# Kernel optimization log

Measured on AMD Instinct MI355X. Metric: run time of the kernel, lower is better.

## Reference

```python
import jax, jax.numpy as jnp
import numpy as np
import jax.scipy.linalg as jsl

K = 4           # num_hops + 1
N = 4096        # nodes
D = 256         # in_dim == out_dim
S = 32          # subspace_dim
ETA = 0.5
EPS = 0.5


def setup_inputs() -> dict:
    key = jax.random.key(0)
    k1, k2, k3 = jax.random.split(key, 3)
    hops = jax.random.normal(k1, (K, N, D), dtype=jnp.float32)
    A = (jax.random.uniform(k2, (N, N)) < 0.01).astype(jnp.float32)
    A = jnp.maximum(A, A.T)
    A = jnp.fill_diagonal(A, 1.0, inplace=False)
    deg = A.sum(axis=1)
    L = jnp.diag(deg) - A  # graph Laplacian
    # orthonormal subspace bases via QR, as in __init__
    raw = jax.random.normal(k3, (K, D, S), dtype=jnp.float32)
    q, _ = jnp.linalg.qr(raw)
    U = q[:, :, :S]
    hop_weights = jnp.ones((K,), dtype=jnp.float32) / K
    threshold = jnp.full((D,), 0.05, dtype=jnp.float32)
    lambda_lap = jnp.asarray(0.1, dtype=jnp.float32)
    return {"hops": hops, "adj_mask": A, "L": L, "U": U,
            "hop_weights": hop_weights, "threshold": threshold,
            "lambda_lap": lambda_lap}


def reference(hops, adj_mask, L, U, hop_weights, threshold, lambda_lap):
    n = hops.shape[1]
    s = U.shape[-1]
    w = jax.nn.softmax(hop_weights, axis=0)
    mask_add = (1.0 - adj_mask) * -1e9  # [n, n]
    I_s = jnp.eye(s, dtype=hops.dtype)
    agg_total = jnp.zeros((hops.shape[2], n), dtype=hops.dtype)  # [d, n]
    coeff = s / (n * EPS ** 2)
    for k in range(K):  # small fixed hop count
        Uk = U[k]                      # [d, s]
        Zk = Uk.T @ hops[k].T          # [s, n]
        M_k = I_s + coeff * (Zk @ Zk.T)  # [s, s]
        cf = jsl.cho_factor(M_k)
        M_inv = jsl.cho_solve(cf, I_s)   # Cholesky inverse
        MZ = M_inv @ Zk                  # [s, n]
        scores = Zk.T @ MZ + mask_add    # [n, n] Mahalanobis-style attention
        alpha = jax.nn.softmax(scores, axis=1)
        grad_k = Uk @ (MZ @ alpha.T)     # [d, n]
        agg_total = agg_total + w[k] * grad_k
    H_agg = agg_total.T                  # [n, d]
    lap_grad = lambda_lap * (L @ H_agg)
    H_half = hops[0] + ETA * H_agg - ETA * lap_grad
    # soft-threshold (proximal step); in_dim == out_dim so no proj
    H_out = jnp.sign(H_half) * jax.nn.relu(jnp.abs(H_half) - threshold[None, :])
    # orthogonality regularizer over subspace bases
    orth_loss = jnp.asarray(0.0, dtype=hops.dtype)
    for k in range(K):
        UkTUk = U[k].T @ U[k]
        orth_loss = orth_loss + ((UkTUk - I_s) ** 2).sum()
        for l in range(k + 1, K):
            orth_loss = orth_loss + ((U[k].T @ U[l]) ** 2).sum()
    lap_smooth = jnp.sum(H_out * (L @ H_out))  # trace(H^T L H)
    return (H_out, orth_loss, lap_smooth, jax.lax.stop_gradient(w))
```

## Files before the change

kernel.cpp:

```cpp
#include <hip/hip_runtime.h>
#include <cstddef>

typedef unsigned short ushortt;
typedef unsigned int uintt;

static constexpr int Nn = 4096;
static constexpr int Dd = 256;
static constexpr int Ss = 32;
static constexpr int Kk = 4;
static constexpr int CAP = 144;
static constexpr int RST = 136;
static constexpr float kEta   = 0.5f;
static constexpr float kCoeff = 0.03125f;

__device__ __forceinline__ float waveReduceSum(float v){
  #pragma unroll
  for (int off = 32; off > 0; off >>= 1) v += __shfl_down(v, off, 64);
  return v;
}
__device__ __forceinline__ float blo(uintt u){ return __uint_as_float(u << 16); }
__device__ __forceinline__ float bhi(uintt u){ return __uint_as_float(u & 0xffff0000u); }
__device__ __forceinline__ ushortt f2b(float x){
  uintt u = __float_as_uint(x);
  uintt r = (u + 0x7fffu + ((u >> 16) & 1u)) >> 16;
  return (ushortt)r;
}
__device__ __forceinline__ float b2f(ushortt u){ return __uint_as_float(((uintt)u) << 16); }

__global__ __launch_bounds__(256) void build_kernel(const float* __restrict__ A,
                                                    const float* __restrict__ hw,
                                                    int* __restrict__ deg,
                                                    int* __restrict__ colx,
                                                    float* __restrict__ out){
  int i = blockIdx.x, tid = threadIdx.x;
  if (i == 0 && tid == 0){
    out[1048576] = 0.f;
    out[1048577] = 0.f;
    float a0=hw[0], a1=hw[1], a2=hw[2], a3=hw[3];
    float mx = fmaxf(fmaxf(a0,a1), fmaxf(a2,a3));
    float e0=expf(a0-mx), e1=expf(a1-mx), e2=expf(a2-mx), e3=expf(a3-mx);
    float s = e0+e1+e2+e3;
    out[1048578]=e0/s; out[1048579]=e1/s; out[1048580]=e2/s; out[1048581]=e3/s;
  }
  int lane = tid & 63, w = tid >> 6;
  __shared__ int wbuf[4][96];
  __shared__ int wcnt[4];
  const float4* row4 = (const float4*)(A + (size_t)i * Nn);
  int cnt = 0;
  int base = w * 256;
  unsigned long long below = (lane == 63) ? 0x7fffffffffffffffull : ((1ull << lane) - 1ull);
  #pragma unroll
  for (int it = 0; it < 4; it++){
    int c4 = base + it * 64 + lane;
    float4 v = row4[c4];
    bool f0 = (v.x != 0.f), f1 = (v.y != 0.f), f2 = (v.z != 0.f), f3 = (v.w != 0.f);
    unsigned long long m0 = __ballot(f0), m1 = __ballot(f1),
                       m2 = __ballot(f2), m3 = __ballot(f3);
    int pre = __popcll(m0 & below) + __popcll(m1 & below)
            + __popcll(m2 & below) + __popcll(m3 & below);
    int pos = cnt + pre;
    int j0 = c4 * 4;
    if (f0){ if (pos < 96) wbuf[w][pos] = j0;     pos++; }
    if (f1){ if (pos < 96) wbuf[w][pos] = j0 + 1; pos++; }
    if (f2){ if (pos < 96) wbuf[w][pos] = j0 + 2; pos++; }
    if (f3){ if (pos < 96) wbuf[w][pos] = j0 + 3; pos++; }
    cnt += __popcll(m0) + __popcll(m1) + __popcll(m2) + __popcll(m3);
  }
  if (cnt > 96) cnt = 96;
  if (lane == 0) wcnt[w] = cnt;
  __syncthreads();
  int off = 0;
  for (int ww = 0; ww < w; ww++) off += wcnt[ww];
  int total = wcnt[0] + wcnt[1] + wcnt[2] + wcnt[3];
  for (int idx = lane; idx < cnt; idx += 64){
    int p = off + idx;
    if (p < CAP) colx[(size_t)i * CAP + p] = wbuf[w][idx];
  }
  if (tid == 0) deg[i] = (total < CAP) ? total : CAP;
}

__global__ __launch_bounds__(256) void z_kernel(const float* __restrict__ hops,
                                                const float* __restrict__ U,
                                                float* __restrict__ Zt4,
                                                float* __restrict__ Ubt){
  int b = blockIdx.x;
  int k = b >> 9;
  int i0 = (b & 511) * 8;
  __shared__ float Us[Ss][260];
  for (int t = threadIdx.x; t < Dd * Ss; t += 256){
    int s = t & 31, d = t >> 5;
    Us[s][d] = U[(size_t)k * Dd * Ss + t];
  }
  __syncthreads();
  int s = threadIdx.x & 31, ii = threadIdx.x >> 5;
  int i = i0 + ii;
  const float4* h4 = (const float4*)(hops + ((size_t)k * Nn + i) * Dd);
  const float4* u4 = (const float4*)(&Us[s][0]);
  float acc = 0.f;
  #pragma unroll 8
  for (int dq = 0; dq < 64; dq++){
    float4 h = h4[dq];
    float4 u = u4[dq];
    acc += h.x*u.x + h.y*u.y + h.z*u.z + h.w*u.w;
  }
  Zt4[(size_t)i * 128 + k * 32 + s] = acc;
  if (b < 128){
    int idx = b * 256 + threadIdx.x;
    int c = idx >> 8, d = idx & 255;
    int kk = c >> 5, s2 = c & 31;
    Ubt[idx] = U[(size_t)kk * Dd * Ss + (size_t)d * Ss + s2];
  }
}

__global__ __launch_bounds__(256) void mpart_kernel(const float* __restrict__ Zt4,
                                                    float* __restrict__ Mpart){
  int b = blockIdx.x;
  int k = b >> 4, ch = b & 15;
  int i0 = ch * 256;
  __shared__ float zs[256][33];
  for (int t = threadIdx.x; t < 256 * 32; t += 256){
    int ii = t >> 5, s = t & 31;
    zs[ii][s] = Zt4[(size_t)(i0 + ii) * 128 + k * 32 + s];
  }
  __syncthreads();
  int tid = threadIdx.x;
  int s2 = tid & 31, s1b = tid >> 5;
  float a0=0.f, a1=0.f, a2=0.f, a3=0.f;
  for (int ii = 0; ii < 256; ii++){
    float zc = zs[ii][s2];
    a0 = fmaf(zs[ii][s1b],      zc, a0);
    a1 = fmaf(zs[ii][8 + s1b],  zc, a1);
    a2 = fmaf(zs[ii][16 + s1b], zc, a2);
    a3 = fmaf(zs[ii][24 + s1b], zc, a3);
  }
  float* outp = Mpart + (size_t)b * 1024;
  outp[0 * 256 + tid] = a0;
  outp[1 * 256 + tid] = a1;
  outp[2 * 256 + tid] = a2;
  outp[3 * 256 + tid] = a3;
}

__global__ __launch_bounds__(256) void inv_kernel(const float* __restrict__ Mpart,
                                                  float* __restrict__ Minv){
  __shared__ float Msh[4][32][33];
  int tid = threadIdx.x;
  for (int e = tid; e < 4096; e += 256){
    int k = e >> 10, rc = e & 1023;
    float s = 0.f;
    for (int ch = 0; ch < 16; ch++) s += Mpart[(size_t)(k * 16 + ch) * 1024 + rc];
    int r = rc >> 5, c = rc & 31;
    Msh[k][r][c] = kCoeff * s + ((r == c) ? 1.f : 0.f);
  }
  __syncthreads();
  int k = tid >> 6, lane = tid & 63, r = lane & 31, half = lane >> 5;
  float a[32];
  #pragma unroll
  for (int j = 0; j < 32; j++) a[j] = half ? ((r == j) ? 1.f : 0.f) : Msh[k][r][j];
  #pragma unroll
  for (int p = 0; p < 32; p++){
    float app = __shfl(a[p], p, 64);
    float pinv = 1.f / app;
    float f = __shfl(a[p], r, 64);
    #pragma unroll
    for (int j = 0; j < 32; j++){
      float pr = __shfl(a[j], p + (half << 5), 64) * pinv;
      a[j] = (r == p) ? pr : fmaf(-f, pr, a[j]);
    }
  }
  if (half){
    #pragma unroll
    for (int j = 0; j < 32; j++) Minv[(size_t)k * 1024 + r * 32 + j] = a[j];
  }
}

__global__ __launch_bounds__(256) void mz_kernel(const float* __restrict__ Zt4,
                                                 const float* __restrict__ Minv,
                                                 ushortt* __restrict__ MZb){
  int b = blockIdx.x;
  int k = b >> 7;
  int i0 = (b & 127) * 32;
  __shared__ float mi[32][33];
  __shared__ float zs[32][33];
  for (int t = threadIdx.x; t < 1024; t += 256){
    int ii = t >> 5, s2 = t & 31;
    mi[ii][s2] = Minv[(size_t)k * 1024 + t];
    zs[ii][s2] = Zt4[(size_t)(i0 + ii) * 128 + k * 32 + s2];
  }
  __syncthreads();
  int s = threadIdx.x & 31;
  for (int rr = 0; rr < 4; rr++){
    int ii = rr * 8 + (threadIdx.x >> 5);
    float acc = 0.f;
    #pragma unroll
    for (int s2 = 0; s2 < 32; s2++) acc = fmaf(mi[s][s2], zs[ii][s2], acc);
    MZb[(size_t)(i0 + ii) * 128 + k * 32 + s] = f2b(acc);
  }
}

__global__ __launch_bounds__(256) void agg_kernel(const float* __restrict__ Zt4,
                                                  const ushortt* __restrict__ MZb,
                                                  const float* __restrict__ wvec,
                                                  const int* __restrict__ deg,
                                                  const int* __restrict__ colx,
                                                  float* __restrict__ Vw){
  int i = blockIdx.x, tid = threadIdx.x;
  int lane = tid & 63, k = tid >> 6;
  __shared__ __align__(16) ushortt rows[CAP * RST];
  __shared__ int cols[CAP];
  __shared__ __align__(16) float zi[128];
  __shared__ float sc[4][CAP + 8];
  int m = deg[i];
  if (tid < 128) zi[tid] = Zt4[(size_t)i * 128 + tid];
  if (tid < m)  cols[tid] = colx[(size_t)i * CAP + tid];
  __syncthreads();

  int q = tid & 3, r = tid >> 2;
  float zq[32];
  {
    const float4* z4 = (const float4*)(&zi[q * 32]);
    #pragma unroll
    for (int p = 0; p < 8; p++){
      float4 z = z4[p];
      zq[p*4+0]=z.x; zq[p*4+1]=z.y; zq[p*4+2]=z.z; zq[p*4+3]=z.w;
    }
  }

  for (int t = r; t < m; t += 64){
    int j = cols[t];
    const uint4* src = (const uint4*)(MZb + (size_t)j * 128 + q * 32);
    uint4 q0 = src[0], q1 = src[1], q2 = src[2], q3 = src[3];
    uint4* dst = (uint4*)(rows + (size_t)t * RST + q * 32);
    dst[0] = q0; dst[1] = q1; dst[2] = q2; dst[3] = q3;
    float acc = 0.f;
    acc += blo(q0.x)*zq[0] + bhi(q0.x)*zq[1] + blo(q0.y)*zq[2] + bhi(q0.y)*zq[3];
    acc += blo(q0.z)*zq[4] + bhi(q0.z)*zq[5] + blo(q0.w)*zq[6] + bhi(q0.w)*zq[7];
    acc += blo(q1.x)*zq[8] + bhi(q1.x)*zq[9] + blo(q1.y)*zq[10]+ bhi(q1.y)*zq[11];
    acc += blo(q1.z)*zq[12]+ bhi(q1.z)*zq[13]+ blo(q1.w)*zq[14]+ bhi(q1.w)*zq[15];
    acc += blo(q2.x)*zq[16]+ bhi(q2.x)*zq[17]+ blo(q2.y)*zq[18]+ bhi(q2.y)*zq[19];
    acc += blo(q2.z)*zq[20]+ bhi(q2.z)*zq[21]+ blo(q2.w)*zq[22]+ bhi(q2.w)*zq[23];
    acc += blo(q3.x)*zq[24]+ bhi(q3.x)*zq[25]+ blo(q3.y)*zq[26]+ bhi(q3.y)*zq[27];
    acc += blo(q3.z)*zq[28]+ bhi(q3.z)*zq[29]+ blo(q3.w)*zq[30]+ bhi(q3.w)*zq[31];
    sc[q][t] = acc;
  }
  __syncthreads();

  float lmax = -3.0e38f;
  for (int t = lane; t < m; t += 64) lmax = fmaxf(lmax, sc[k][t]);
  #pragma unroll
  for (int off = 32; off > 0; off >>= 1) lmax = fmaxf(lmax, __shfl_xor(lmax, off, 64));
  float lsum = 0.f;
  for (int t = lane; t < m; t += 64){
    float e = __expf(sc[k][t] - lmax);
    sc[k][t] = e;
    lsum += e;
  }
  #pragma unroll
  for (int off = 32; off > 0; off >>= 1) lsum += __shfl_xor(lsum, off, 64);
  float scale = wvec[k] / lsum;

  int c2 = lane & 15, h = lane >> 4;
  float a0 = 0.f, a1 = 0.f;
  #pragma unroll 4
  for (int t = h; t < m; t += 4){
    uintt u = *(const uintt*)(rows + (size_t)t * RST + k * 32 + c2 * 2);
    float e = sc[k][t];
    a0 = fmaf(blo(u), e, a0);
    a1 = fmaf(bhi(u), e, a1);
  }
  a0 += __shfl_xor(a0, 16, 64); a0 += __shfl_xor(a0, 32, 64);
  a1 += __shfl_xor(a1, 16, 64); a1 += __shfl_xor(a1, 32, 64);
  if (h == 0){
    float2 v2 = make_float2(a0 * scale, a1 * scale);
    *(float2*)(Vw + (size_t)i * 128 + k * 32 + c2 * 2) = v2;
  }
}

__global__ __launch_bounds__(256) void gatherv_kernel(const float* __restrict__ Vw,
                                                      const float* __restrict__ lam_ptr,
                                                      const int* __restrict__ deg,
                                                      const int* __restrict__ colx,
                                                      float* __restrict__ cVc){
  int i = blockIdx.x, tid = threadIdx.x;
  int c = tid & 127, g = tid >> 7;
  __shared__ int cols[CAP];
  __shared__ float vred[2][128];
  int m = deg[i];
  if (tid < m) cols[tid] = colx[(size_t)i * CAP + tid];
  __syncthreads();
  float acc = 0.f;
  #pragma unroll 8
  for (int t = g; t < m; t += 2)
    acc += Vw[(size_t)cols[t] * 128 + c];
  vred[g][c] = acc;
  __syncthreads();
  if (tid < 128){
    float nb = vred[0][tid] + vred[1][tid];
    float lam = lam_ptr[0];
    float self = Vw[(size_t)i * 128 + tid];
    cVc[(size_t)i * 128 + tid] = kEta * (1.f - lam * (float)m) * self + kEta * lam * nb;
  }
}

__global__ __launch_bounds__(256) void houtblend_kernel(const float* __restrict__ cVc,
                                                        const float* __restrict__ Ubt,
                                                        const float* __restrict__ hops0,
                                                        const float* __restrict__ thr,
                                                        const float* __restrict__ U,
                                                        float* __restrict__ out,
                                                        ushortt* __restrict__ Hb){
  int tid = threadIdx.x;
  if (blockIdx.x >= 256){
    int g = (blockIdx.x - 256) * 256 + tid;
    int pair = g >> 10;
    int idx = g & 1023;
    int s1 = idx >> 5, s2 = idx & 31;
    const int pk_[10] = {0,0,0,0,1,1,1,2,2,3};
    const int pl_[10] = {0,1,2,3,1,2,3,2,3,3};
    int pk = pk_[pair], pl = pl_[pair];
    const float* Uk = U + (size_t)pk * Dd * Ss;
    const float* Ul = U + (size_t)pl * Dd * Ss;
    float dot = 0.f;
    for (int d = 0; d < Dd; d++) dot += Uk[d * Ss + s1] * Ul[d * Ss + s2];
    float val = dot - ((pk == pl && s1 == s2) ? 1.f : 0.f);
    val *= val;
    val = waveReduceSum(val);
    __shared__ float redo[4];
    if ((tid & 63) == 0) redo[tid >> 6] = val;
    __syncthreads();
    if (tid == 0) atomicAdd(out + 1048576, redo[0] + redo[1] + redo[2] + redo[3]);
    return;
  }
  int i0 = blockIdx.x * 16;
  __shared__ float Cs[16][132];
  for (int t = tid; t < 16 * 128; t += 256){
    int ii = t >> 7, c = t & 127;
    Cs[ii][c] = cVc[(size_t)(i0 + ii) * 128 + c];
  }
  __syncthreads();
  int d4 = tid & 63, g = tid >> 6;
  float4 acc[4];
  #pragma unroll
  for (int r = 0; r < 4; r++) acc[r] = make_float4(0.f, 0.f, 0.f, 0.f);
  #pragma unroll 2
  for (int c = 0; c < 128; c++){
    float4 ub = ((const float4*)(Ubt + (size_t)c * 256))[d4];
    #pragma unroll
    for (int r = 0; r < 4; r++){
      float cs = Cs[g * 4 + r][c];
      acc[r].x = fmaf(cs, ub.x, acc[r].x);
      acc[r].y = fmaf(cs, ub.y, acc[r].y);
      acc[r].z = fmaf(cs, ub.z, acc[r].z);
      acc[r].w = fmaf(cs, ub.w, acc[r].w);
    }
  }
  float4 th = ((const float4*)thr)[d4];
  #pragma unroll
  for (int r = 0; r < 4; r++){
    int i = i0 + g * 4 + r;
    float4 hp = ((const float4*)(hops0 + (size_t)i * 256))[d4];
    float hx = hp.x + acc[r].x, hy = hp.y + acc[r].y;
    float hz = hp.z + acc[r].z, hw = hp.w + acc[r].w;
    float4 o;
    o.x = copysignf(fmaxf(fabsf(hx) - th.x, 0.f), hx);
    o.y = copysignf(fmaxf(fabsf(hy) - th.y, 0.f), hy);
    o.z = copysignf(fmaxf(fabsf(hz) - th.z, 0.f), hz);
    o.w = copysignf(fmaxf(fabsf(hw) - th.w, 0.f), hw);
    ((float4*)(out + (size_t)i * 256))[d4] = o;
    ushort4 hb;
    hb.x = f2b(o.x); hb.y = f2b(o.y); hb.z = f2b(o.z); hb.w = f2b(o.w);
    *((ushort4*)(Hb + (size_t)i * 256 + d4 * 4)) = hb;
  }
}

__global__ __launch_bounds__(256) void lap_kernel(const float* __restrict__ Hout,
                                                  const ushortt* __restrict__ Hb,
                                                  const int* __restrict__ deg,
                                                  const int* __restrict__ colx,
                                                  float* __restrict__ lap_part){
  int b = blockIdx.x;
  int i = b >> 1, half = b & 1;
  int tid = threadIdx.x;
  int dl = tid & 127, g = tid >> 7;
  int d = half * 128 + dl;
  __shared__ int cols[CAP];
  int m = deg[i];
  if (tid < m) cols[tid] = colx[(size_t)i * CAP + tid];
  __syncthreads();
  float nb = 0.f;
  #pragma unroll 8
  for (int t = g; t < m; t += 2)
    nb += b2f(Hb[(size_t)cols[t] * 256 + d]);
  float hi = Hout[(size_t)i * 256 + d];
  float part = -hi * nb;
  if (g == 0) part = fmaf((float)m * hi, hi, part);
  part = waveReduceSum(part);
  __shared__ float red[4];
  if ((tid & 63) == 0) red[tid >> 6] = part;
  __syncthreads();
  if (tid == 0) lap_part[b] = red[0] + red[1] + red[2] + red[3];
}

__global__ __launch_bounds__(256) void lapred_kernel(const float* __restrict__ lap_part,
                                                     float* __restrict__ out){
  int tid = threadIdx.x;
  float s = 0.f;
  const float4* p4 = (const float4*)lap_part;
  #pragma unroll
  for (int q = 0; q < 8; q++){
    float4 v = p4[q * 256 + tid];
    s += v.x + v.y + v.z + v.w;
  }
  s = waveReduceSum(s);
  __shared__ float red[4];
  if ((tid & 63) == 0) red[tid >> 6] = s;
  __syncthreads();
  if (tid == 0) out[1048577] = red[0] + red[1] + red[2] + red[3];
}

extern "C" void kernel_launch(void* const* d_in, const int* in_sizes, int n_in,
                              void* d_out, int out_size, void* d_ws, size_t ws_size,
                              hipStream_t stream)
{
  const float* hops = (const float*)d_in[0];
  const float* A    = (const float*)d_in[1];
  const float* L    = (const float*)d_in[2];
  const float* U    = (const float*)d_in[3];
  const float* hw   = (const float*)d_in[4];
  const float* thr  = (const float*)d_in[5];
  const float* lam  = (const float*)d_in[6];
  (void)L; (void)in_sizes; (void)n_in; (void)out_size; (void)ws_size;

  float* out = (float*)d_out;
  float* ws  = (float*)d_ws;

  float*   Zt4   = ws;
  float*   Vw    = ws + 524288;
  float*   cVc   = ws + 1048576;
  ushortt* MZb   = (ushortt*)(ws + 1572864);
  ushortt* Hb    = (ushortt*)(ws + 1835008);
  float*   Ubt   = ws + 2359296;
  float*   Mpart = ws + 2392064;
  float*   Minv  = ws + 2457600;
  int*     deg   = (int*)(ws + 2461696);
  int*     colx  = (int*)(ws + 2465792);
  float*   lapp  = ws + 3121152;

  float* w_out = out + 1048578;

  build_kernel    <<<Nn, 256, 0, stream>>>(A, hw, deg, colx, out);
  z_kernel        <<<Kk*512, 256, 0, stream>>>(hops, U, Zt4, Ubt);
  mpart_kernel    <<<Kk*16, 256, 0, stream>>>(Zt4, Mpart);
  inv_kernel      <<<1, 256, 0, stream>>>(Mpart, Minv);
  mz_kernel       <<<Kk*128, 256, 0, stream>>>(Zt4, Minv, MZb);
  agg_kernel      <<<Nn, 256, 0, stream>>>(Zt4, MZb, w_out, deg, colx, Vw);
  gatherv_kernel  <<<Nn, 256, 0, stream>>>(Vw, lam, deg, colx, cVc);
  houtblend_kernel<<<296, 256, 0, stream>>>(cVc, Ubt, hops, thr, U, out, Hb);
  lap_kernel      <<<2*Nn, 256, 0, stream>>>(out, Hb, deg, colx, lapp);
  lapred_kernel   <<<1, 256, 0, stream>>>(lapp, out);
}
```

Baseline: 303.2 us.

## Fuse build with Z projection, gather with blend, and lap reduction via last-block

Merges the adjacency-build and Z-projection kernels into one launch that splits work by block index. Folds the neighbor gather of Vw into the output blend kernel, so each block handles 4 rows and the cVc intermediate buffer is no longer needed. Replaces the separate lap reduction launch with an atomic done-counter that lets the last lap block do the final sum. This removes three kernel launches and one global round trip. In exchange the blend kernel runs with less per-block row reuse of Ubt and gets more blocks, and the reduction now relies on an atomic counter.

```diff
diff --git a/kernel.cpp b/kernel.cpp
--- a/kernel.cpp
+++ b/kernel.cpp
@@ -27,15 +27,52 @@
 }
 __device__ __forceinline__ float b2f(ushortt u){ return __uint_as_float(((uintt)u) << 16); }
 
-__global__ __launch_bounds__(256) void build_kernel(const float* __restrict__ A,
-                                                    const float* __restrict__ hw,
-                                                    int* __restrict__ deg,
-                                                    int* __restrict__ colx,
-                                                    float* __restrict__ out){
-  int i = blockIdx.x, tid = threadIdx.x;
+__global__ __launch_bounds__(256) void buildz_kernel(const float* __restrict__ A,
+                                                     const float* __restrict__ hw,
+                                                     const float* __restrict__ hops,
+                                                     const float* __restrict__ U,
+                                                     int* __restrict__ deg,
+                                                     int* __restrict__ colx,
+                                                     float* __restrict__ Zt4,
+                                                     float* __restrict__ Ubt,
+                                                     int* __restrict__ done_ctr,
+                                                     float* __restrict__ out){
+  int tid = threadIdx.x;
+  if (blockIdx.x >= Nn){
+    int b = blockIdx.x - Nn;
+    int k = b >> 9;
+    int i0 = (b & 511) * 8;
+    __shared__ float Us[Ss][260];
+    for (int t = tid; t < Dd * Ss; t += 256){
+      int s = t & 31, d = t >> 5;
+      Us[s][d] = U[(size_t)k * Dd * Ss + t];
+    }
+    __syncthreads();
+    int s = tid & 31, ii = tid >> 5;
+    int i = i0 + ii;
+    const float4* h4 = (const float4*)(hops + ((size_t)k * Nn + i) * Dd);
+    const float4* u4 = (const float4*)(&Us[s][0]);
+    float acc = 0.f;
+    #pragma unroll 8
+    for (int dq = 0; dq < 64; dq++){
+      float4 h = h4[dq];
+      float4 u = u4[dq];
+      acc += h.x*u.x + h.y*u.y + h.z*u.z + h.w*u.w;
+    }
+    Zt4[(size_t)i * 128 + k * 32 + s] = acc;
+    if (b < 128){
+      int idx = b * 256 + tid;
+      int c = idx >> 8, d = idx & 255;
+      int kk = c >> 5, s2 = c & 31;
+      Ubt[idx] = U[(size_t)kk * Dd * Ss + (size_t)d * Ss + s2];
+    }
+    return;
+  }
+  int i = blockIdx.x;
   if (i == 0 && tid == 0){
     out[1048576] = 0.f;
     out[1048577] = 0.f;
+    *done_ctr = 0;
     float a0=hw[0], a1=hw[1], a2=hw[2], a3=hw[3];
     float mx = fmaxf(fmaxf(a0,a1), fmaxf(a2,a3));
     float e0=expf(a0-mx), e1=expf(a1-mx), e2=expf(a2-mx), e3=expf(a3-mx);
@@ -77,39 +114,6 @@
     if (p < CAP) colx[(size_t)i * CAP + p] = wbuf[w][idx];
   }
   if (tid == 0) deg[i] = (total < CAP) ? total : CAP;
-}
-
-__global__ __launch_bounds__(256) void z_kernel(const float* __restrict__ hops,
-                                                const float* __restrict__ U,
-                                                float* __restrict__ Zt4,
-                                                float* __restrict__ Ubt){
-  int b = blockIdx.x;
-  int k = b >> 9;
-  int i0 = (b & 511) * 8;
-  __shared__ float Us[Ss][260];
-  for (int t = threadIdx.x; t < Dd * Ss; t += 256){
-    int s = t & 31, d = t >> 5;
-    Us[s][d] = U[(size_t)k * Dd * Ss + t];
-  }
-  __syncthreads();
-  int s = threadIdx.x & 31, ii = threadIdx.x >> 5;
-  int i = i0 + ii;
-  const float4* h4 = (const float4*)(hops + ((size_t)k * Nn + i) * Dd);
-  const float4* u4 = (const float4*)(&Us[s][0]);
-  float acc = 0.f;
-  #pragma unroll 8
-  for (int dq = 0; dq < 64; dq++){
-    float4 h = h4[dq];
-    float4 u = u4[dq];
-    acc += h.x*u.x + h.y*u.y + h.z*u.z + h.w*u.w;
-  }
-  Zt4[(size_t)i * 128 + k * 32 + s] = acc;
-  if (b < 128){
-    int idx = b * 256 + threadIdx.x;
-    int c = idx >> 8, d = idx & 255;
-    int kk = c >> 5, s2 = c & 31;
-    Ubt[idx] = U[(size_t)kk * Dd * Ss + (size_t)d * Ss + s2];
-  }
 }
 
 __global__ __launch_bounds__(256) void mpart_kernel(const float* __restrict__ Zt4,
@@ -275,42 +279,19 @@
   }
 }
 
-__global__ __launch_bounds__(256) void gatherv_kernel(const float* __restrict__ Vw,
-                                                      const float* __restrict__ lam_ptr,
-                                                      const int* __restrict__ deg,
-                                                      const int* __restrict__ colx,
-                                                      float* __restrict__ cVc){
-  int i = blockIdx.x, tid = threadIdx.x;
-  int c = tid & 127, g = tid >> 7;
-  __shared__ int cols[CAP];
-  __shared__ float vred[2][128];
-  int m = deg[i];
-  if (tid < m) cols[tid] = colx[(size_t)i * CAP + tid];
-  __syncthreads();
-  float acc = 0.f;
-  #pragma unroll 8
-  for (int t = g; t < m; t += 2)
-    acc += Vw[(size_t)cols[t] * 128 + c];
-  vred[g][c] = acc;
-  __syncthreads();
-  if (tid < 128){
-    float nb = vred[0][tid] + vred[1][tid];
-    float lam = lam_ptr[0];
-    float self = Vw[(size_t)i * 128 + tid];
-    cVc[(size_t)i * 128 + tid] = kEta * (1.f - lam * (float)m) * self + kEta * lam * nb;
-  }
-}
-
-__global__ __launch_bounds__(256) void houtblend_kernel(const float* __restrict__ cVc,
-                                                        const float* __restrict__ Ubt,
-                                                        const float* __restrict__ hops0,
-                                                        const float* __restrict__ thr,
-                                                        const float* __restrict__ U,
-                                                        float* __restrict__ out,
-                                                        ushortt* __restrict__ Hb){
+__global__ __launch_bounds__(256) void gho_kernel(const float* __restrict__ Vw,
+                                                  const float* __restrict__ Ubt,
+                                                  const float* __restrict__ hops0,
+                                                  const float* __restrict__ thr,
+                                                  const float* __restrict__ U,
+                                                  const float* __restrict__ lam_ptr,
+                                                  const int* __restrict__ deg,
+                                                  const int* __restrict__ colx,
+                                                  float* __restrict__ out,
+                                                  ushortt* __restrict__ Hb){
   int tid = threadIdx.x;
-  if (blockIdx.x >= 256){
-    int g = (blockIdx.x - 256) * 256 + tid;
+  if (blockIdx.x >= 1024){
+    int g = (blockIdx.x - 1024) * 256 + tid;
     int pair = g >> 10;
     int idx = g & 1023;
     int s1 = idx >> 5, s2 = idx & 31;
@@ -330,59 +311,80 @@
     if (tid == 0) atomicAdd(out + 1048576, redo[0] + redo[1] + redo[2] + redo[3]);
     return;
   }
-  int i0 = blockIdx.x * 16;
-  __shared__ float Cs[16][132];
-  for (int t = tid; t < 16 * 128; t += 256){
-    int ii = t >> 7, c = t & 127;
-    Cs[ii][c] = cVc[(size_t)(i0 + ii) * 128 + c];
+  int i0 = blockIdx.x * 4;
+  int lane = tid & 63, w = tid >> 6;
+  __shared__ float Cs[4][132];
+  __shared__ int cols_s[4][CAP];
+  {
+    int i = i0 + w;
+    int m = deg[i];
+    for (int t = lane; t < m; t += 64) cols_s[w][t] = colx[(size_t)i * CAP + t];
+    float lam = lam_ptr[0];
+    int half = lane >> 5, c32 = lane & 31;
+    float4 acc = make_float4(0.f, 0.f, 0.f, 0.f);
+    for (int t = half; t < m; t += 2){
+      int j = cols_s[w][t];
+      float4 v = ((const float4*)(Vw + (size_t)j * 128))[c32];
+      acc.x += v.x; acc.y += v.y; acc.z += v.z; acc.w += v.w;
+    }
+    acc.x += __shfl_xor(acc.x, 32, 64);
+    acc.y += __shfl_xor(acc.y, 32, 64);
+    acc.z += __shfl_xor(acc.z, 32, 64);
+    acc.w += __shfl_xor(acc.w, 32, 64);
+    if (half == 0){
+      float4 self = ((const float4*)(Vw + (size_t)i * 128))[c32];
+      float ca = kEta * (1.f - lam * (float)m);
+      float cb = kEta * lam;
+      float4 o;
+      o.x = fmaf(ca, self.x, cb * acc.x);
+      o.y = fmaf(ca, self.y, cb * acc.y);
+      o.z = fmaf(ca, self.z, cb * acc.z);
+      o.w = fmaf(ca, self.w, cb * acc.w);
+      *(float4*)(&Cs[w][c32 * 4]) = o;
+    }
   }
   __syncthreads();
   int d4 = tid & 63, g = tid >> 6;
-  float4 acc[4];
-  #pragma unroll
-  for (int r = 0; r < 4; r++) acc[r] = make_float4(0.f, 0.f, 0.f, 0.f);
-  #pragma unroll 2
+  float4 acc = make_float4(0.f, 0.f, 0.f, 0.f);
+  #pragma unroll 4
   for (int c = 0; c < 128; c++){
     float4 ub = ((const float4*)(Ubt + (size_t)c * 256))[d4];
-    #pragma unroll
-    for (int r = 0; r < 4; r++){
-      float cs = Cs[g * 4 + r][c];
-      acc[r].x = fmaf(cs, ub.x, acc[r].x);
-      acc[r].y = fmaf(cs, ub.y, acc[r].y);
-      acc[r].z = fmaf(cs, ub.z, acc[r].z);
-      acc[r].w = fmaf(cs, ub.w, acc[r].w);
-    }
+    float cs = Cs[g][c];
+    acc.x = fmaf(cs, ub.x, acc.x);
+    acc.y = fmaf(cs, ub.y, acc.y);
+    acc.z = fmaf(cs, ub.z, acc.z);
+    acc.w = fmaf(cs, ub.w, acc.w);
   }
   float4 th = ((const float4*)thr)[d4];
-  #pragma unroll
-  for (int r = 0; r < 4; r++){
-    int i = i0 + g * 4 + r;
-    float4 hp = ((const float4*)(hops0 + (size_t)i * 256))[d4];
-    float hx = hp.x + acc[r].x, hy = hp.y + acc[r].y;
-    float hz = hp.z + acc[r].z, hw = hp.w + acc[r].w;
-    float4 o;
-    o.x = copysignf(fmaxf(fabsf(hx) - th.x, 0.f), hx);
-    o.y = copysignf(fmaxf(fabsf(hy) - th.y, 0.f), hy);
-    o.z = copysignf(fmaxf(fabsf(hz) - th.z, 0.f), hz);
-    o.w = copysignf(fmaxf(fabsf(hw) - th.w, 0.f), hw);
-    ((float4*)(out + (size_t)i * 256))[d4] = o;
-    ushort4 hb;
-    hb.x = f2b(o.x); hb.y = f2b(o.y); hb.z = f2b(o.z); hb.w = f2b(o.w);
-    *((ushort4*)(Hb + (size_t)i * 256 + d4 * 4)) = hb;
-  }
+  int i = i0 + g;
+  float4 hp = ((const float4*)(hops0 + (size_t)i * 256))[d4];
+  float hx = hp.x + acc.x, hy = hp.y + acc.y;
+  float hz = hp.z + acc.z, hw = hp.w + acc.w;
+  float4 o;
+  o.x = copysignf(fmaxf(fabsf(hx) - th.x, 0.f), hx);
+  o.y = copysignf(fmaxf(fabsf(hy) - th.y, 0.f), hy);
+  o.z = copysignf(fmaxf(fabsf(hz) - th.z, 0.f), hz);
+  o.w = copysignf(fmaxf(fabsf(hw) - th.w, 0.f), hw);
+  ((float4*)(out + (size_t)i * 256))[d4] = o;
+  ushort4 hb;
+  hb.x = f2b(o.x); hb.y = f2b(o.y); hb.z = f2b(o.z); hb.w = f2b(o.w);
+  *((ushort4*)(Hb + (size_t)i * 256 + d4 * 4)) = hb;
 }
 
 __global__ __launch_bounds__(256) void lap_kernel(const float* __restrict__ Hout,
                                                   const ushortt* __restrict__ Hb,
                                                   const int* __restrict__ deg,
                                                   const int* __restrict__ colx,
-                                                  float* __restrict__ lap_part){
+                                                  float* __restrict__ lap_part,
+                                                  int* __restrict__ done_ctr,
+                                                  float* __restrict__ out){
   int b = blockIdx.x;
   int i = b >> 1, half = b & 1;
   int tid = threadIdx.x;
   int dl = tid & 127, g = tid >> 7;
   int d = half * 128 + dl;
   __shared__ int cols[CAP];
+  __shared__ bool last_s;
   int m = deg[i];
   if (tid < m) cols[tid] = colx[(size_t)i * CAP + tid];
   __syncthreads();
@@ -397,24 +399,23 @@
   __shared__ float red[4];
   if ((tid & 63) == 0) red[tid >> 6] = part;
   __syncthreads();
-  if (tid == 0) lap_part[b] = red[0] + red[1] + red[2] + red[3];
-}
-
-__global__ __launch_bounds__(256) void lapred_kernel(const float* __restrict__ lap_part,
-                                                     float* __restrict__ out){
-  int tid = threadIdx.x;
-  float s = 0.f;
-  const float4* p4 = (const float4*)lap_part;
-  #pragma unroll
-  for (int q = 0; q < 8; q++){
-    float4 v = p4[q * 256 + tid];
-    s += v.x + v.y + v.z + v.w;
-  }
-  s = waveReduceSum(s);
-  __shared__ float red[4];
-  if ((tid & 63) == 0) red[tid >> 6] = s;
-  __syncthreads();
-  if (tid == 0) out[1048577] = red[0] + red[1] + red[2] + red[3];
+  if (tid == 0){
+    float bs = red[0] + red[1] + red[2] + red[3];
+    __hip_atomic_store(&lap_part[b], bs, __ATOMIC_RELAXED, __HIP_MEMORY_SCOPE_AGENT);
+    int old = __hip_atomic_fetch_add(done_ctr, 1, __ATOMIC_ACQ_REL, __HIP_MEMORY_SCOPE_AGENT);
+    last_s = (old == 2 * Nn - 1);
+  }
+  __syncthreads();
+  if (last_s){
+    float s = 0.f;
+    for (int qv = tid; qv < 2 * Nn; qv += 256)
+      s += __hip_atomic_load(&lap_part[qv], __ATOMIC_RELAXED, __HIP_MEMORY_SCOPE_AGENT);
+    s = waveReduceSum(s);
+    __shared__ float redl[4];
+    if ((tid & 63) == 0) redl[tid >> 6] = s;
+    __syncthreads();
+    if (tid == 0) out[1048577] = redl[0] + redl[1] + redl[2] + redl[3];
+  }
 }
 
 extern "C" void kernel_launch(void* const* d_in, const int* in_sizes, int n_in,
@@ -435,7 +436,6 @@
 
   float*   Zt4   = ws;
   float*   Vw    = ws + 524288;
-  float*   cVc   = ws + 1048576;
   ushortt* MZb   = (ushortt*)(ws + 1572864);
   ushortt* Hb    = (ushortt*)(ws + 1835008);
   float*   Ubt   = ws + 2359296;
@@ -444,17 +444,15 @@
   int*     deg   = (int*)(ws + 2461696);
   int*     colx  = (int*)(ws + 2465792);
   float*   lapp  = ws + 3121152;
+  int*     dctr  = (int*)(ws + 3129344);
 
   float* w_out = out + 1048578;
 
-  build_kernel    <<<Nn, 256, 0, stream>>>(A, hw, deg, colx, out);
-  z_kernel        <<<Kk*512, 256, 0, stream>>>(hops, U, Zt4, Ubt);
-  mpart_kernel    <<<Kk*16, 256, 0, stream>>>(Zt4, Mpart);
-  inv_kernel      <<<1, 256, 0, stream>>>(Mpart, Minv);
-  mz_kernel       <<<Kk*128, 256, 0, stream>>>(Zt4, Minv, MZb);
-  agg_kernel      <<<Nn, 256, 0, stream>>>(Zt4, MZb, w_out, deg, colx, Vw);
-  gatherv_kernel  <<<Nn, 256, 0, stream>>>(Vw, lam, deg, colx, cVc);
-  houtblend_kernel<<<296, 256, 0, stream>>>(cVc, Ubt, hops, thr, U, out, Hb);
-  lap_kernel      <<<2*Nn, 256, 0, stream>>>(out, Hb, deg, colx, lapp);
-  lapred_kernel   <<<1, 256, 0, stream>>>(lapp, out);
-}
+  buildz_kernel<<<Nn + Kk*512, 256, 0, stream>>>(A, hw, hops, U, deg, colx, Zt4, Ubt, dctr, out);
+  mpart_kernel <<<Kk*16, 256, 0, stream>>>(Zt4, Mpart);
+  inv_kernel   <<<1, 256, 0, stream>>>(Mpart, Minv);
+  mz_kernel    <<<Kk*128, 256, 0, stream>>>(Zt4, Minv, MZb);
+  agg_kernel   <<<Nn, 256, 0, stream>>>(Zt4, MZb, w_out, deg, colx, Vw);
+  gho_kernel   <<<1064, 256, 0, stream>>>(Vw, Ubt, hops, thr, U, lam, deg, colx, out, Hb);
+  lap_kernel   <<<2*Nn, 256, 0, stream>>>(out, Hb, deg, colx, lapp, dctr, out);
+}
```

Result: slower. 441.2 us (+45.5%).
